# Optimization experiments

Hardware: AMD Instinct MI355X
Metric: run time of the kernel (lower is better)

Reference implementation:

```python
import jax, jax.numpy as jnp
import numpy as np
from jax import lax

B, N, S, K = 16, 8192, 1024, 32
FACTOR = 1.0
EPS_BN = 1e-5


def farthest_point_sample(xyz, npoint):
    # xyz: [B, N, 3] -> idx [B, npoint]. Deterministic start at index 0
    # (torch version starts at a random index; start choice doesn't change the math pattern).
    b, n, _ = xyz.shape
    bidx = jnp.arange(b)

    def step(carry, _):
        distance, farthest = carry
        centroid = xyz[bidx, farthest]                      # [B, 3]
        dist = jnp.sum((xyz - centroid[:, None, :]) ** 2, -1)  # [B, N]
        distance = jnp.minimum(distance, dist)
        new_far = jnp.argmax(distance, axis=-1)
        return (distance, new_far), farthest

    init = (jnp.full((b, n), 1e10, xyz.dtype), jnp.zeros((b,), jnp.int32))
    _, idxs = lax.scan(step, init, None, length=npoint)
    return idxs.T  # [B, npoint]


def square_distance(src, dst):
    # [B,Ns,3] x [B,Nd,3] -> [B,Ns,Nd]
    d = -2.0 * jnp.einsum('bnc,bmc->bnm', src, dst)
    d += jnp.sum(src ** 2, -1)[:, :, None]
    d += jnp.sum(dst ** 2, -1)[:, None, :]
    return d


def safe_cdist(x):
    # x: [B, C, S]; pairwise euclidean over rows -> [B, C, C]; zero-safe sqrt
    diff = x[:, :, None, :] - x[:, None, :, :]          # [B, C, C, S]
    sq = jnp.sum(diff * diff, -1)
    pos = sq > 0
    return jnp.where(pos, jnp.sqrt(jnp.where(pos, sq, 1.0)), 0.0)


def batchnorm(x, gamma, beta, axes):
    mean = jnp.mean(x, axes, keepdims=True)
    var = jnp.var(x, axes, keepdims=True)  # biased, as in torch BN normalization
    return (x - mean) / jnp.sqrt(var + EPS_BN) * gamma + beta


def reference(xyz, bn1_gamma, bn1_beta, bn2_gamma, bn2_beta):
    b = xyz.shape[0]
    # --- FPS sampling ---
    fps_idx = farthest_point_sample(lax.stop_gradient(xyz), S)          # [B,S]
    new_xyz = jnp.take_along_axis(xyz, fps_idx[:, :, None], axis=1)     # [B,S,3]
    # --- kNN grouping ---
    sq = square_distance(lax.stop_gradient(new_xyz), lax.stop_gradient(xyz))  # [B,S,N]
    _, knn_idx = lax.top_k(-sq, K)                                      # [B,S,K] indices
    grouped = jax.vmap(lambda p, i: p[i])(xyz, knn_idx)                 # [B,S,K,3]
    diff = grouped - new_xyz[:, :, None, :]
    std = jnp.std(diff, ddof=1)                                         # scalar, unbiased like torch.std
    knn_norm = diff / (std + 1e-5)
    center = jnp.broadcast_to(new_xyz[:, :, None, :], (b, S, K, 3))
    knn_xyz = jnp.concatenate([knn_norm, center], axis=-1)              # [B,S,K,6]
    # --- Pooling over neighbors ---
    x = jnp.transpose(knn_xyz, (0, 3, 1, 2))                            # [B,6,S,K]
    lc = jnp.max(x, -1) + jnp.mean(x, -1)                               # [B,6,S]
    lc = jax.nn.relu(batchnorm(lc, bn1_gamma[None, :, None], bn1_beta[None, :, None], (0, 2)))
    # --- Consecutive representation (cdist + superdiagonal factor) ---
    tfcw = safe_cdist(lc)                                               # [B,6,6]
    i = jnp.arange(5)
    tfcw = tfcw.at[:, i, i + 1].multiply(FACTOR)
    # --- Pooling2 ---
    feat = tfcw.reshape(b, -1)                                          # [B,36]
    feat = jax.nn.relu(batchnorm(feat, bn2_gamma[None, :], bn2_beta[None, :], (0,)))
    return feat


def setup_inputs() -> dict:
    key = jax.random.key(0)
    k1, = jax.random.split(key, 1)
    return {
        'xyz': jax.random.normal(k1, (B, N, 3), dtype=jnp.float32),
        'bn1_gamma': jnp.ones((6,), jnp.float32),
        'bn1_beta': jnp.zeros((6,), jnp.float32),
        'bn2_gamma': jnp.ones((36,), jnp.float32),
        'bn2_beta': jnp.zeros((36,), jnp.float32),
    }
```

## Files before the change

### kernel.cpp

```cpp
#include <hip/hip_runtime.h>
#include <hip/hip_bf16.h>

constexpr int BB = 16;
constexpr int NN = 8192;
constexpr int SS = 1024;
constexpr int KK = 32;
constexpr int BUFC = 256;

__device__ __forceinline__ float b2f(__hip_bfloat16 h) { return __bfloat162float(h); }

__device__ __forceinline__ unsigned mkey32(float d) {
    unsigned u = __float_as_uint(d);
    return u ^ (0x80000000u | (unsigned)((int)u >> 31));
}

__device__ __forceinline__ unsigned long long dist_key(const float* __restrict__ pb,
                                                       int idx, float qx, float qy,
                                                       float qz, float qq) {
    float px = pb[idx * 3 + 0];
    float py = pb[idx * 3 + 1];
    float pz = pb[idx * 3 + 2];
    float dot = __fadd_rn(__fadd_rn(__fmul_rn(qx, px), __fmul_rn(qy, py)), __fmul_rn(qz, pz));
    float pp  = __fadd_rn(__fadd_rn(__fmul_rn(px, px), __fmul_rn(py, py)), __fmul_rn(pz, pz));
    float d = __fadd_rn(__fadd_rn(__fmul_rn(-2.0f, dot), qq), pp);
    return ((unsigned long long)mkey32(d) << 32) | (unsigned)idx;
}

template <int CTRL, int RMASK>
__device__ __forceinline__ unsigned long long dppmove_u64(unsigned long long v) {
    int lo = (int)(unsigned)v, hi = (int)(unsigned)(v >> 32);
    int nlo = __builtin_amdgcn_update_dpp(lo, lo, CTRL, RMASK, 0xf, false);
    int nhi = __builtin_amdgcn_update_dpp(hi, hi, CTRL, RMASK, 0xf, false);
    return ((unsigned long long)(unsigned)nhi << 32) | (unsigned)nlo;
}

__device__ __forceinline__ unsigned long long u64max(unsigned long long a,
                                                     unsigned long long b) {
    return a > b ? a : b;
}

__device__ __forceinline__ unsigned long long wave_max_dpp(unsigned long long k) {
    k = u64max(k, dppmove_u64<0x121, 0xf>(k));
    k = u64max(k, dppmove_u64<0x122, 0xf>(k));
    k = u64max(k, dppmove_u64<0x124, 0xf>(k));
    k = u64max(k, dppmove_u64<0x128, 0xf>(k));
    k = u64max(k, dppmove_u64<0x142, 0xa>(k));
    k = u64max(k, dppmove_u64<0x143, 0xc>(k));
    return k;
}

__device__ __forceinline__ unsigned long long bitonic64(unsigned long long v, int lane) {
#pragma unroll
    for (int k = 2; k <= 64; k <<= 1) {
#pragma unroll
        for (int j = k >> 1; j > 0; j >>= 1) {
            unsigned long long p = __shfl_xor(v, j);
            bool up = ((lane & k) == 0);
            bool lower = ((lane & j) == 0);
            bool take_min = (up == lower);
            v = take_min ? (p < v ? p : v) : (p > v ? p : v);
        }
    }
    return v;
}

__global__ __launch_bounds__(256) void convert_kernel(
    const void* __restrict__ xyz_raw, const void* __restrict__ g1r,
    const void* __restrict__ b1r, const void* __restrict__ g2r,
    const void* __restrict__ b2r, float* __restrict__ xyzf,
    float* __restrict__ params, void* __restrict__ out_raw) {
    const unsigned short* u = (const unsigned short*)xyz_raw;
    unsigned short s = u[2 * (threadIdx.x & 63)];
    int e = (s >> 7) & 0xFF;
    unsigned long long m = __ballot(e >= 100 && e <= 140);
    bool isbf = __popcll(m) > 48;

    const int NT = BB * NN * 3;
    int tid = blockIdx.x * blockDim.x + threadIdx.x;
    int stride = gridDim.x * blockDim.x;
    if (isbf) {
        const __hip_bfloat16* p = (const __hip_bfloat16*)xyz_raw;
        for (int i = tid; i < NT; i += stride) xyzf[i] = b2f(p[i]);
    } else {
        const float* p = (const float*)xyz_raw;
        for (int i = tid; i < NT; i += stride) xyzf[i] = p[i];
    }
    if (blockIdx.x == 0 && threadIdx.x < 85) {
        int t = threadIdx.x;
        if (t == 84) {
            params[84] = isbf ? 1.0f : 0.0f;
        } else {
            const void* src; int off;
            if (t < 6)       { src = g1r; off = t; }
            else if (t < 12) { src = b1r; off = t - 6; }
            else if (t < 48) { src = g2r; off = t - 12; }
            else             { src = b2r; off = t - 48; }
            params[t] = isbf ? b2f(((const __hip_bfloat16*)src)[off])
                             : ((const float*)src)[off];
        }
    }
    if (blockIdx.x == 1 && threadIdx.x < 64) {
        for (int i = threadIdx.x; i < 576; i += 64) {
            if (isbf) ((__hip_bfloat16*)out_raw)[i] = __float2bfloat16(1.0f);
            else      ((float*)out_raw)[i] = 1.0f;
        }
    }
}

__global__ __attribute__((amdgpu_flat_work_group_size(512, 512)))
__attribute__((amdgpu_waves_per_eu(2, 2)))
void fps_kernel(const float* __restrict__ xyzf, float* __restrict__ new_xyz) {
    constexpr int T = 512, P = NN / T;
    const int b = blockIdx.x, t = threadIdx.x;
    const float* xb = xyzf + (size_t)b * NN * 3;

    __shared__ float sxyz[NN * 3];
    __shared__ unsigned long long skey[2][8];

    float px[P], py[P], pz[P], ds[P];
#pragma unroll
    for (int j = 0; j < P; j++) {
        int p = t + j * T;
        px[j] = xb[p * 3 + 0];
        py[j] = xb[p * 3 + 1];
        pz[j] = xb[p * 3 + 2];
        ds[j] = 1e10f;
    }
    for (int i = t; i < NN * 3; i += T) sxyz[i] = xb[i];

    float cx = xb[0], cy = xb[1], cz = xb[2];
    if (t == 0) {
        float* o = new_xyz + (size_t)b * SS * 3;
        o[0] = cx; o[1] = cy; o[2] = cz;
    }
    const int wave = t >> 6, lane = t & 63;
    __syncthreads();

    for (int step = 1; step < SS; step++) {
        float bv = -1.0f; int bj = 0;
#pragma unroll
        for (int j = 0; j < P; j++) {
            float dx = __fsub_rn(px[j], cx);
            float dy = __fsub_rn(py[j], cy);
            float dz = __fsub_rn(pz[j], cz);
            float d = __fadd_rn(__fadd_rn(__fmul_rn(dx, dx), __fmul_rn(dy, dy)), __fmul_rn(dz, dz));
            float mm = fminf(ds[j], d);
            ds[j] = mm;
            if (mm > bv) { bv = mm; bj = j; }
        }
        unsigned idx = (unsigned)(t + bj * T);
        unsigned long long key =
            ((unsigned long long)__float_as_uint(bv) << 32) | (unsigned)(~idx);

        key = wave_max_dpp(key);
        const int par = step & 1;
        if (lane == 63) skey[par][wave] = key;
        __syncthreads();

        unsigned long long k0 = u64max(skey[par][0], skey[par][1]);
        unsigned long long k1 = u64max(skey[par][2], skey[par][3]);
        unsigned long long k2 = u64max(skey[par][4], skey[par][5]);
        unsigned long long k3 = u64max(skey[par][6], skey[par][7]);
        unsigned long long bk = u64max(u64max(k0, k1), u64max(k2, k3));

        unsigned gidx = ~(unsigned)bk;
        cx = sxyz[gidx * 3 + 0];
        cy = sxyz[gidx * 3 + 1];
        cz = sxyz[gidx * 3 + 2];
        if (t == 0) {
            float* o = new_xyz + ((size_t)b * SS + step) * 3;
            o[0] = cx; o[1] = cy; o[2] = cz;
        }
    }
}

__global__ __launch_bounds__(256, 2) void knn_kernel(const float* __restrict__ xyzf,
                                                     const float* __restrict__ new_xyz,
                                                     float* __restrict__ A,
                                                     double* __restrict__ qstats) {
    __shared__ unsigned long long buf[4][BUFC];
    const int t = threadIdx.x;
    const int lane = t & 63, wv = t >> 6;
    const int w = blockIdx.x * 4 + wv;
    const int b = w >> 10, s = w & 1023;

    const float* q = new_xyz + ((size_t)b * SS + s) * 3;
    float qx = q[0], qy = q[1], qz = q[2];
    float qq = __fadd_rn(__fadd_rn(__fmul_rn(qx, qx), __fmul_rn(qy, qy)), __fmul_rn(qz, qz));

    const float* pb = xyzf + (size_t)b * NN * 3;
    const unsigned long long ltmask = (1ull << lane) - 1ull;

    unsigned long long lmin = ~0ull;
    for (int j = 0; j < 128; j++) {
        unsigned long long key = dist_key(pb, j * 64 + lane, qx, qy, qz, qq);
        lmin = key < lmin ? key : lmin;
    }

    unsigned long long vs = bitonic64(lmin, lane);
    unsigned long long That = __shfl(vs, 31);

    for (int i = lane; i < BUFC; i += 64) buf[wv][i] = ~0ull;
    int base = 0;
    for (int j = 0; j < 128; j++) {
        unsigned long long key = dist_key(pb, j * 64 + lane, qx, qy, qz, qq);
        bool f = key <= That;
        unsigned long long bal = __ballot(f);
        int pos = base + __popcll(bal & ltmask);
        if (f && pos < BUFC) buf[wv][pos] = key;
        base += __popcll(bal);
    }

    if (base > BUFC) {
        unsigned lo = 0, hi = (unsigned)(That >> 32);
        for (int it = 0; it < 32; it++) {
            unsigned mid = lo + ((hi - lo) >> 1);
            int c = 0;
            for (int j = 0; j < 128; j++) {
                unsigned long long key = dist_key(pb, j * 64 + lane, qx, qy, qz, qq);
                c += ((unsigned)(key >> 32) <= mid) ? 1 : 0;
            }
#pragma unroll
            for (int o = 32; o > 0; o >>= 1) c += __shfl_xor(c, o);
            if (c >= 32) hi = mid; else lo = mid + 1;
        }
        That = ((unsigned long long)hi << 32) | 0xFFFFFFFFull;
        for (int i = lane; i < BUFC; i += 64) buf[wv][i] = ~0ull;
        base = 0;
        for (int j = 0; j < 128; j++) {
            unsigned long long key = dist_key(pb, j * 64 + lane, qx, qy, qz, qq);
            bool f = key <= That;
            unsigned long long bal = __ballot(f);
            int pos = base + __popcll(bal & ltmask);
            if (f && pos < BUFC) buf[wv][pos] = key;
            base += __popcll(bal);
        }
        if (base > BUFC) base = BUFC;
    }

    int M = base;
    unsigned long long kept = ~0ull;
    if (M <= 64) {
        unsigned long long v = (lane < M) ? buf[wv][lane] : ~0ull;
        v = bitonic64(v, lane);
        kept = v;
    } else {
        unsigned long long c0 = buf[wv][lane];
        unsigned long long c1 = buf[wv][64 + lane];
        unsigned long long c2 = buf[wv][128 + lane];
        unsigned long long c3 = buf[wv][192 + lane];
        for (int r = 0; r < KK; r++) {
            unsigned long long m01 = c0 < c1 ? c0 : c1;
            unsigned long long m23 = c2 < c3 ? c2 : c3;
            unsigned long long mm = m01 < m23 ? m01 : m23;
#pragma unroll
            for (int o = 32; o > 0; o >>= 1) {
                unsigned long long t2 = __shfl_xor(mm, o);
                mm = t2 < mm ? t2 : mm;
            }
            if (lane == r) kept = mm;
            c0 = (c0 == mm) ? ~0ull : c0;
            c1 = (c1 == mm) ? ~0ull : c1;
            c2 = (c2 == mm) ? ~0ull : c2;
            c3 = (c3 == mm) ? ~0ull : c3;
        }
    }

    bool act = (lane < KK);
    float gx = 0.0f, gy = 0.0f, gz = 0.0f;
    if (act) {
        unsigned nidx = (unsigned)kept;
        gx = pb[nidx * 3 + 0];
        gy = pb[nidx * 3 + 1];
        gz = pb[nidx * 3 + 2];
    }
    float dx = __fsub_rn(gx, qx);
    float dy = __fsub_rn(gy, qy);
    float dz = __fsub_rn(gz, qz);
    float mx = act ? dx : -3.402823466e38f;
    float my = act ? dy : -3.402823466e38f;
    float mz = act ? dz : -3.402823466e38f;
    float sx = act ? dx : 0.0f;
    float sy = act ? dy : 0.0f;
    float sz = act ? dz : 0.0f;
    double s1 = act ? ((double)dx + (double)dy + (double)dz) : 0.0;
    double s2 = act ? ((double)dx * dx + (double)dy * dy + (double)dz * dz) : 0.0;
#pragma unroll
    for (int o = 32; o > 0; o >>= 1) {
        mx = fmaxf(mx, __shfl_xor(mx, o));
        my = fmaxf(my, __shfl_xor(my, o));
        mz = fmaxf(mz, __shfl_xor(mz, o));
        sx += __shfl_xor(sx, o);
        sy += __shfl_xor(sy, o);
        sz += __shfl_xor(sz, o);
        s1 += __shfl_xor(s1, o);
        s2 += __shfl_xor(s2, o);
    }
    if (lane == 0) {
        float* a = A + ((size_t)b * SS + s) * 3;
        a[0] = __fadd_rn(mx, __fmul_rn(sx, 0.03125f));
        a[1] = __fadd_rn(my, __fmul_rn(sy, 0.03125f));
        a[2] = __fadd_rn(mz, __fmul_rn(sz, 0.03125f));
        qstats[2 * w + 0] = s1;
        qstats[2 * w + 1] = s2;
    }
}

__global__ __launch_bounds__(256) void reduce_stats_kernel(const double* __restrict__ qstats,
                                                           double* __restrict__ stats) {
    __shared__ double r1[4], r2[4];
    int t = threadIdx.x;
    double a = 0.0, bsum = 0.0;
    for (int i = t; i < BB * SS; i += 256) { a += qstats[2 * i]; bsum += qstats[2 * i + 1]; }
#pragma unroll
    for (int o = 32; o > 0; o >>= 1) { a += __shfl_xor(a, o); bsum += __shfl_xor(bsum, o); }
    int wv = t >> 6, ln = t & 63;
    if (ln == 0) { r1[wv] = a; r2[wv] = bsum; }
    __syncthreads();
    if (t == 0) {
        stats[0] = r1[0] + r1[1] + r1[2] + r1[3];
        stats[1] = r2[0] + r2[1] + r2[2] + r2[3];
    }
}

__global__ __launch_bounds__(256) void lc_kernel(const float* __restrict__ new_xyz,
                                                 const float* __restrict__ A,
                                                 const double* __restrict__ stats,
                                                 float* __restrict__ lc,
                                                 double* __restrict__ bn1acc) {
    __shared__ double red[4];
    const int b = blockIdx.x / 6, c = blockIdx.x % 6;
    const int t = threadIdx.x;
    const double n = (double)BB * SS * KK * 3;
    double sd = stats[0], sq = stats[1];
    double var = (sq - sd * sd / n) / (n - 1.0);
    float stdv = (float)sqrt(var);
    float denom = __fadd_rn(stdv, 1e-5f);

    double s1 = 0.0, s2 = 0.0;
    for (int r = 0; r < 4; r++) {
        int s = r * 256 + t;
        float v;
        if (c < 3) {
            v = A[((size_t)b * SS + s) * 3 + c] / denom;
        } else {
            float ww = new_xyz[((size_t)b * SS + s) * 3 + (c - 3)];
            v = __fadd_rn(ww, ww);
        }
        lc[((size_t)b * 6 + c) * SS + s] = v;
        s1 += (double)v;
        s2 += (double)v * (double)v;
    }
#pragma unroll
    for (int off = 32; off > 0; off >>= 1) { s1 += __shfl_down(s1, off); s2 += __shfl_down(s2, off); }
    int wv = t >> 6, ln = t & 63;
    if (ln == 0) red[wv] = s1;
    __syncthreads();
    if (t == 0) atomicAdd(&bn1acc[c * 2 + 0], red[0] + red[1] + red[2] + red[3]);
    __syncthreads();
    if (ln == 0) red[wv] = s2;
    __syncthreads();
    if (t == 0) atomicAdd(&bn1acc[c * 2 + 1], red[0] + red[1] + red[2] + red[3]);
}

__global__ __launch_bounds__(256) void cdist_kernel(const float* __restrict__ lc,
                                                    const double* __restrict__ bn1acc,
                                                    const float* __restrict__ params,
                                                    float* __restrict__ tf) {
    __shared__ float sy[6 * SS];
    const int b = blockIdx.x, t = threadIdx.x;
    float mean[6], sde[6], gg[6], bt[6];
    const double n = (double)BB * SS;
#pragma unroll
    for (int c = 0; c < 6; c++) {
        double m = bn1acc[c * 2 + 0] / n;
        double v = bn1acc[c * 2 + 1] / n - m * m;
        mean[c] = (float)m;
        sde[c] = sqrtf((float)v + 1e-5f);
        gg[c] = params[c];
        bt[c] = params[6 + c];
    }
    for (int r = 0; r < 24; r++) {
        int g = r * 256 + t;
        int c = g >> 10;
        float v = lc[(size_t)b * 6 * SS + g];
        float y = (v - mean[c]) / sde[c] * gg[c] + bt[c];
        sy[g] = fmaxf(y, 0.0f);
    }
    __syncthreads();
    if (t < 6) tf[b * 36 + t * 7] = 0.0f;

    const int w = t >> 6, lane = t & 63;
    const int PI[15] = {0,0,0,0,0,1,1,1,1,2,2,2,3,3,4};
    const int PJ[15] = {1,2,3,4,5,2,3,4,5,3,4,5,4,5,5};
    for (int r = 0; r < 4; r++) {
        int p = w + r * 4;
        if (p < 15) {
            int i = PI[p], j = PJ[p];
            float acc = 0.0f;
            for (int m2 = 0; m2 < 16; m2++) {
                int s = lane + m2 * 64;
                float d = sy[i * SS + s] - sy[j * SS + s];
                acc += d * d;
            }
#pragma unroll
            for (int off = 32; off > 0; off >>= 1) acc += __shfl_down(acc, off);
            if (lane == 0) {
                float v = acc > 0.0f ? sqrtf(acc) : 0.0f;
                const float FACTOR = 1.0f;
                tf[b * 36 + i * 6 + j] = (j == i + 1) ? v * FACTOR : v;
                tf[b * 36 + j * 6 + i] = v;
            }
        }
    }
}

__global__ __launch_bounds__(64) void bn2_kernel(const float* __restrict__ tf,
                                                 const float* __restrict__ params,
                                                 void* __restrict__ out_raw) {
    int f = threadIdx.x;
    if (f >= 36) return;
    bool isbf = params[84] != 0.0f;
    float x[16]; float sum = 0.0f;
#pragma unroll
    for (int b = 0; b < 16; b++) { x[b] = tf[b * 36 + f]; sum += x[b]; }
    float mean = sum * 0.0625f;
    float vs = 0.0f;
#pragma unroll
    for (int b = 0; b < 16; b++) { float d = x[b] - mean; vs += d * d; }
    float var = vs * 0.0625f;
    float denom = sqrtf(var + 1e-5f);
    float g = params[12 + f], bb = params[48 + f];
#pragma unroll
    for (int b = 0; b < 16; b++) {
        float y = (x[b] - mean) / denom * g + bb;
        y = fmaxf(y, 0.0f);
        if (isbf) ((__hip_bfloat16*)out_raw)[b * 36 + f] = __float2bfloat16(y);
        else      ((float*)out_raw)[b * 36 + f] = y;
    }
}

extern "C" void kernel_launch(void* const* d_in, const int* in_sizes, int n_in,
                              void* d_out, int out_size, void* d_ws, size_t ws_size,
                              hipStream_t stream) {
    const void* xyz_raw = d_in[0];
    const void* g1r = d_in[1]; const void* b1r = d_in[2];
    const void* g2r = d_in[3]; const void* b2r = d_in[4];
    {
        const void* six[2] = {nullptr, nullptr}; int n6 = 0;
        const void* t36[2] = {nullptr, nullptr}; int n36 = 0;
        const void* big = nullptr;
        for (int i = 0; i < n_in; i++) {
            if (in_sizes[i] == BB * NN * 3) big = d_in[i];
            else if (in_sizes[i] == 6  && n6  < 2) six[n6++]  = d_in[i];
            else if (in_sizes[i] == 36 && n36 < 2) t36[n36++] = d_in[i];
        }
        if (big && n6 == 2 && n36 == 2) {
            xyz_raw = big; g1r = six[0]; b1r = six[1]; g2r = t36[0]; b2r = t36[1];
        }
    }

    char* ws = (char*)d_ws;
    float* xyzf    = (float*)(ws + 0);
    float* new_xyz = (float*)(ws + 1572864);
    float* A       = (float*)(ws + 1769472);
    float* lc      = (float*)(ws + 1966080);
    float* tf      = (float*)(ws + 2359296);
    double* stats  = (double*)(ws + 2361600);
    double* bn1acc = stats + 2;
    float* params  = (float*)(ws + 2361712);
    double* qstats = (double*)(ws + 2362112);

    hipMemsetAsync(stats, 0, 14 * sizeof(double), stream);
    hipLaunchKernelGGL(convert_kernel, dim3(512), dim3(256), 0, stream,
                       xyz_raw, g1r, b1r, g2r, b2r, xyzf, params, d_out);
    hipLaunchKernelGGL(fps_kernel,          dim3(16),   dim3(512), 0, stream, xyzf, new_xyz);
    hipLaunchKernelGGL(knn_kernel,          dim3(4096), dim3(256), 0, stream, xyzf, new_xyz, A, qstats);
    hipLaunchKernelGGL(reduce_stats_kernel, dim3(1),    dim3(256), 0, stream, qstats, stats);
    hipLaunchKernelGGL(lc_kernel,           dim3(96),   dim3(256), 0, stream, new_xyz, A, stats, lc, bn1acc);
    hipLaunchKernelGGL(cdist_kernel,        dim3(16),   dim3(256), 0, stream, lc, bn1acc, params, tf);
    hipLaunchKernelGGL(bn2_kernel,          dim3(1),    dim3(64),  0, stream, tf, params, d_out);

    (void)in_sizes; (void)n_in; (void)out_size; (void)ws_size;
}
```

Measured before the change: 1.192 ms.

## Morton-sort FPS points per thread and skip updates via bounding-box pruning

Result: no change. 1.183 ms (-0.8%).

```diff
diff --git a/kernel.cpp b/kernel.cpp
--- a/kernel.cpp
+++ b/kernel.cpp
@@ -34,19 +34,21 @@
     return ((unsigned long long)(unsigned)nhi << 32) | (unsigned)nlo;
 }
 
-__device__ __forceinline__ unsigned long long u64max(unsigned long long a,
-                                                     unsigned long long b) {
-    return a > b ? a : b;
-}
-
-__device__ __forceinline__ unsigned long long wave_max_dpp(unsigned long long k) {
-    k = u64max(k, dppmove_u64<0x121, 0xf>(k));
-    k = u64max(k, dppmove_u64<0x122, 0xf>(k));
-    k = u64max(k, dppmove_u64<0x124, 0xf>(k));
-    k = u64max(k, dppmove_u64<0x128, 0xf>(k));
-    k = u64max(k, dppmove_u64<0x142, 0xa>(k));
-    k = u64max(k, dppmove_u64<0x143, 0xc>(k));
-    return k;
+template <int CTRL, int RMASK>
+__device__ __forceinline__ double dppmax_f64(double v) {
+    double m = __longlong_as_double(
+        dppmove_u64<CTRL, RMASK>((unsigned long long)__double_as_longlong(v)));
+    return fmax(v, m);
+}
+
+__device__ __forceinline__ double wave_max_dpp_f64(double v) {
+    v = dppmax_f64<0x121, 0xf>(v);
+    v = dppmax_f64<0x122, 0xf>(v);
+    v = dppmax_f64<0x124, 0xf>(v);
+    v = dppmax_f64<0x128, 0xf>(v);
+    v = dppmax_f64<0x142, 0xa>(v);
+    v = dppmax_f64<0x143, 0xc>(v);
+    return v;
 }
 
 __device__ __forceinline__ unsigned long long bitonic64(unsigned long long v, int lane) {
@@ -61,6 +63,15 @@
             v = take_min ? (p < v ? p : v) : (p > v ? p : v);
         }
     }
+    return v;
+}
+
+__device__ __forceinline__ unsigned expand3(unsigned v) {
+    v &= 0x3FFu;
+    v = (v | (v << 16)) & 0x030000FFu;
+    v = (v | (v << 8))  & 0x0300F00Fu;
+    v = (v | (v << 4))  & 0x030C30C3u;
+    v = (v | (v << 2))  & 0x09249249u;
     return v;
 }
 
@@ -115,18 +126,95 @@
     const float* xb = xyzf + (size_t)b * NN * 3;
 
     __shared__ float sxyz[NN * 3];
-    __shared__ unsigned long long skey[2][8];
+    __shared__ unsigned sortk[NN];
+    __shared__ double skey[2][8];
+    __shared__ float sred[6][8];
+    __shared__ float sbb[6];
+
+    for (int i = t; i < NN * 3; i += T) sxyz[i] = xb[i];
+    __syncthreads();
+
+    {
+        float mn[3] = {3.4e38f, 3.4e38f, 3.4e38f};
+        float mx[3] = {-3.4e38f, -3.4e38f, -3.4e38f};
+        for (int j = 0; j < P; j++) {
+            int p = t + j * T;
+#pragma unroll
+            for (int c = 0; c < 3; c++) {
+                float v = sxyz[p * 3 + c];
+                mn[c] = fminf(mn[c], v);
+                mx[c] = fmaxf(mx[c], v);
+            }
+        }
+#pragma unroll
+        for (int o = 32; o > 0; o >>= 1) {
+#pragma unroll
+            for (int c = 0; c < 3; c++) {
+                mn[c] = fminf(mn[c], __shfl_xor(mn[c], o));
+                mx[c] = fmaxf(mx[c], __shfl_xor(mx[c], o));
+            }
+        }
+        int wv = t >> 6, ln = t & 63;
+        if (ln == 0) {
+#pragma unroll
+            for (int c = 0; c < 3; c++) { sred[c][wv] = mn[c]; sred[3 + c][wv] = mx[c]; }
+        }
+        __syncthreads();
+        if (t < 6) {
+            bool ismin = t < 3;
+            float v = sred[t][0];
+            for (int w = 1; w < 8; w++) v = ismin ? fminf(v, sred[t][w]) : fmaxf(v, sred[t][w]);
+            sbb[t] = v;
+        }
+        __syncthreads();
+    }
+
+    {
+        float bx = sbb[0], by = sbb[1], bz = sbb[2];
+        float qsx = 63.0f / fmaxf(sbb[3] - bx, 1e-9f);
+        float qsy = 63.0f / fmaxf(sbb[4] - by, 1e-9f);
+        float qsz = 63.0f / fmaxf(sbb[5] - bz, 1e-9f);
+        for (int p = t; p < NN; p += T) {
+            unsigned qx = (unsigned)min(63, (int)((sxyz[p * 3 + 0] - bx) * qsx));
+            unsigned qy = (unsigned)min(63, (int)((sxyz[p * 3 + 1] - by) * qsy));
+            unsigned qz = (unsigned)min(63, (int)((sxyz[p * 3 + 2] - bz) * qsz));
+            unsigned m = (expand3(qx) << 2) | (expand3(qy) << 1) | expand3(qz);
+            sortk[p] = (m << 13) | (unsigned)p;
+        }
+        __syncthreads();
+        for (unsigned k = 2; k <= (unsigned)NN; k <<= 1) {
+            for (unsigned j = k >> 1; j > 0; j >>= 1) {
+#pragma unroll
+                for (int r = 0; r < NN / 2 / T; r++) {
+                    unsigned gid = (unsigned)(r * T + t);
+                    unsigned i = ((gid & ~(j - 1)) << 1) | (gid & (j - 1));
+                    unsigned p2 = i | j;
+                    unsigned a = sortk[i], c2 = sortk[p2];
+                    bool up = ((i & k) == 0);
+                    if ((a > c2) == up) { sortk[i] = c2; sortk[p2] = a; }
+                }
+                __syncthreads();
+            }
+        }
+    }
 
     float px[P], py[P], pz[P], ds[P];
+    int nidx[P];
+    float lox = 3.4e38f, loy = 3.4e38f, loz = 3.4e38f;
+    float hix = -3.4e38f, hiy = -3.4e38f, hiz = -3.4e38f;
 #pragma unroll
     for (int j = 0; j < P; j++) {
-        int p = t + j * T;
-        px[j] = xb[p * 3 + 0];
-        py[j] = xb[p * 3 + 1];
-        pz[j] = xb[p * 3 + 2];
+        unsigned oi = sortk[t * P + j] & 8191u;
+        float x = sxyz[oi * 3 + 0];
+        float y = sxyz[oi * 3 + 1];
+        float z = sxyz[oi * 3 + 2];
+        px[j] = x; py[j] = y; pz[j] = z;
         ds[j] = 1e10f;
-    }
-    for (int i = t; i < NN * 3; i += T) sxyz[i] = xb[i];
+        nidx[j] = (int)~oi;
+        lox = fminf(lox, x); hix = fmaxf(hix, x);
+        loy = fminf(loy, y); hiy = fmaxf(hiy, y);
+        loz = fminf(loz, z); hiz = fmaxf(hiz, z);
+    }
 
     float cx = xb[0], cy = xb[1], cz = xb[2];
     if (t == 0) {
@@ -134,36 +222,45 @@
         o[0] = cx; o[1] = cy; o[2] = cz;
     }
     const int wave = t >> 6, lane = t & 63;
-    __syncthreads();
+
+    double bk = 0.0;
+    float tb = 1e10f;
 
     for (int step = 1; step < SS; step++) {
-        float bv = -1.0f; int bj = 0;
-#pragma unroll
-        for (int j = 0; j < P; j++) {
-            float dx = __fsub_rn(px[j], cx);
-            float dy = __fsub_rn(py[j], cy);
-            float dz = __fsub_rn(pz[j], cz);
-            float d = __fadd_rn(__fadd_rn(__fmul_rn(dx, dx), __fmul_rn(dy, dy)), __fmul_rn(dz, dz));
-            float mm = fminf(ds[j], d);
-            ds[j] = mm;
-            if (mm > bv) { bv = mm; bj = j; }
-        }
-        unsigned idx = (unsigned)(t + bj * T);
-        unsigned long long key =
-            ((unsigned long long)__float_as_uint(bv) << 32) | (unsigned)(~idx);
-
-        key = wave_max_dpp(key);
+        float ax = fmaxf(fmaxf(__fsub_rn(lox, cx), __fsub_rn(cx, hix)), 0.0f);
+        float ay = fmaxf(fmaxf(__fsub_rn(loy, cy), __fsub_rn(cy, hiy)), 0.0f);
+        float az = fmaxf(fmaxf(__fsub_rn(loz, cz), __fsub_rn(cz, hiz)), 0.0f);
+        float lbd = ax * ax + ay * ay + az * az;
+        if (lbd * 0.999f < tb) {
+            double nbk = 0.0;
+#pragma unroll
+            for (int j = 0; j < P; j++) {
+                float dx = __fsub_rn(px[j], cx);
+                float dy = __fsub_rn(py[j], cy);
+                float dz = __fsub_rn(pz[j], cz);
+                float d = __fadd_rn(__fadd_rn(__fmul_rn(dx, dx), __fmul_rn(dy, dy)),
+                                    __fmul_rn(dz, dz));
+                float mm = fminf(ds[j], d);
+                ds[j] = mm;
+                double kk = __hiloint2double(__float_as_int(mm), nidx[j]);
+                nbk = fmax(nbk, kk);
+            }
+            bk = nbk;
+            tb = __uint_as_float((unsigned)__double2hiint(bk));
+        }
+
+        double wk = wave_max_dpp_f64(bk);
         const int par = step & 1;
-        if (lane == 63) skey[par][wave] = key;
+        if (lane == 63) skey[par][wave] = wk;
         __syncthreads();
 
-        unsigned long long k0 = u64max(skey[par][0], skey[par][1]);
-        unsigned long long k1 = u64max(skey[par][2], skey[par][3]);
-        unsigned long long k2 = u64max(skey[par][4], skey[par][5]);
-        unsigned long long k3 = u64max(skey[par][6], skey[par][7]);
-        unsigned long long bk = u64max(u64max(k0, k1), u64max(k2, k3));
-
-        unsigned gidx = ~(unsigned)bk;
+        double k0 = fmax(skey[par][0], skey[par][1]);
+        double k1 = fmax(skey[par][2], skey[par][3]);
+        double k2 = fmax(skey[par][4], skey[par][5]);
+        double k3 = fmax(skey[par][6], skey[par][7]);
+        double bkk = fmax(fmax(k0, k1), fmax(k2, k3));
+
+        unsigned gidx = ~(unsigned)(unsigned long long)__double_as_longlong(bkk);
         cx = sxyz[gidx * 3 + 0];
         cy = sxyz[gidx * 3 + 1];
         cz = sxyz[gidx * 3 + 2];
```
